# Performance work log

Hardware: AMD Instinct MI355X
Metric: run time of the kernel (lower is better)

Reference implementation:

```python
import jax, jax.numpy as jnp
import numpy as np

NUM_EXPERTS = 8
TOP_K = 2
HIDDEN = 768
INTERMEDIATE = 3072
NUM_TOKENS = 8192


def setup_inputs() -> dict:
    key = jax.random.key(0)
    k0, k1, k2, k3 = jax.random.split(key, 4)
    hidden_states = jax.random.normal(k0, (NUM_TOKENS, HIDDEN), dtype=jnp.float32)
    router_weight = jax.random.normal(k1, (NUM_EXPERTS, HIDDEN), dtype=jnp.float32) * 0.02
    w1 = jax.random.normal(k2, (NUM_EXPERTS, INTERMEDIATE, HIDDEN), dtype=jnp.float32) * 0.02
    w2 = jax.random.normal(k3, (NUM_EXPERTS, HIDDEN, INTERMEDIATE), dtype=jnp.float32) * 0.02
    bias = jnp.zeros((HIDDEN,), dtype=jnp.float32)
    return {"hidden_states": hidden_states, "router_weight": router_weight,
            "w1": w1, "w2": w2, "bias": bias}


def _moe_forward(hidden_states, router_weight, w1, w2, bias):
    T, H = hidden_states.shape
    E = w1.shape[0]
    # Router: ReplicatedLinear(H, E, bias=False)
    logits = hidden_states @ router_weight.T                      # [T, E]
    # fused_topk: softmax over all experts, then top-k, renormalize=False
    probs = jax.nn.softmax(logits, axis=-1)                       # [T, E]
    topk_w, topk_ids = jax.lax.top_k(probs, TOP_K)                # [T, K]
    # per-token per-expert combine weight (top-k ids are distinct)
    gates = jnp.sum(jax.nn.one_hot(topk_ids, E, dtype=probs.dtype) * topk_w[..., None], axis=1)  # [T, E]
    # Expert MLP: y_e = gelu(x @ w1[e].T) @ w2[e].T  (non-gated, activation_without_mul('gelu'))
    out = jnp.zeros_like(hidden_states)
    for e in range(E):  # small fixed expert count
        h = jax.nn.gelu(hidden_states @ w1[e].T, approximate=False)  # [T, I]
        out = out + gates[:, e:e + 1] * (h @ w2[e].T)                # [T, H]
    return out + bias


def reference(hidden_states, router_weight, w1, w2, bias):
    return _moe_forward(hidden_states, router_weight, w1, w2, bias)
```

## Files before the change

kernel.cpp:

```cpp
#include <hip/hip_runtime.h>
#include <hip/hip_bf16.h>
#include <math.h>

#define NT 8192
#define HD 768
#define ID 3072
#define NE 8
#define BK 32
#define MAXB 72
#define ASZ (256 * BK)
#define BSZ (128 * BK)
#define RT_BLOCKS 256
#define CW1_BLOCKS (NE * ID * HD / 4 / 1024)
#define G1_GEMM (MAXB * (ID / 128))
#define CW2_BLOCKS (NE * HD * ID / 4 / 2048)

typedef __bf16 bf16x8 __attribute__((ext_vector_type(8)));
typedef float f32x4 __attribute__((ext_vector_type(4)));

__device__ __forceinline__ unsigned short f2bf(float f) {
    union { float f; unsigned u; } v; v.f = f;
    unsigned r = v.u + 0x7FFFu + ((v.u >> 16) & 1u);
    return (unsigned short)(r >> 16);
}
__device__ __forceinline__ float bf2f(unsigned short b) {
    union { unsigned u; float f; } v; v.u = ((unsigned)b) << 16;
    return v.f;
}
__device__ __forceinline__ unsigned cvt_pk_bf16(float lo, float hi) {
    unsigned r;
    asm("v_cvt_pk_bf16_f32 %0, %1, %2" : "=v"(r) : "v"(lo), "v"(hi));
    return r;
}
__device__ __forceinline__ float gelu_s(float v) {
    float z = v * (1.5957691216057308f + 0.07135481283687945f * v * v);
    float e = __expf(-z);
    return v * __builtin_amdgcn_rcpf(1.0f + e);
}

__device__ __forceinline__ void gload16(const void* g, void* l) {
    auto* lds = reinterpret_cast<__attribute__((address_space(3))) unsigned int*>(
        reinterpret_cast<uintptr_t>(l));
    auto* gp = reinterpret_cast<const __attribute__((address_space(1))) unsigned int*>(
        reinterpret_cast<uintptr_t>(g));
    __builtin_amdgcn_global_load_lds(gp, lds, 16, 0, 0);
}

__device__ __forceinline__ void decode_em(const int* counts, int bsw, int& e, int& m0) {
    e = -1; m0 = 0;
    int s = 0;
#pragma unroll
    for (int q = 0; q < NE; q++) {
        int nb = (counts[q] + 255) >> 8;
        if (bsw >= s && bsw < s + nb) { e = q; m0 = (bsw - s) << 8; }
        s += nb;
    }
}

__global__ void k_front(const float* __restrict__ x, const float* __restrict__ rw,
                        const float4* __restrict__ w1, ushort4* __restrict__ w1b,
                        ushort4* __restrict__ xb4, float* __restrict__ gates,
                        uchar2* __restrict__ choice) {
    __shared__ float rws[NE * HD];
    const int tid = threadIdx.x;
    if (blockIdx.x >= RT_BLOCKS) {
        int base = (blockIdx.x - RT_BLOCKS) * 1024 + tid;
#pragma unroll
        for (int i = 0; i < 4; i++) {
            int idx = base + i * 256;
            float4 a = w1[idx];
            ushort4 ra;
            ra.x = f2bf(a.x); ra.y = f2bf(a.y); ra.z = f2bf(a.z); ra.w = f2bf(a.w);
            w1b[idx] = ra;
        }
        return;
    }
    for (int i = tid; i < NE * HD / 4; i += 256)
        ((float4*)rws)[i] = ((const float4*)rw)[i];
    __syncthreads();
    const int wid = tid >> 6, lane = tid & 63;
    const float4* rws4 = (const float4*)rws;
    for (int it = 0; it < 8; ++it) {
        const int t = blockIdx.x * 32 + wid * 8 + it;
        const float4* xp4 = (const float4*)(x + (size_t)t * HD);
        float acc[NE];
#pragma unroll
        for (int e = 0; e < NE; e++) acc[e] = 0.f;
#pragma unroll
        for (int j = 0; j < HD / 256; j++) {
            float4 v = xp4[lane + 64 * j];
            ushort4 o;
            o.x = f2bf(v.x); o.y = f2bf(v.y); o.z = f2bf(v.z); o.w = f2bf(v.w);
            xb4[(size_t)t * (HD / 4) + lane + 64 * j] = o;
#pragma unroll
            for (int e = 0; e < NE; e++) {
                float4 w = rws4[e * (HD / 4) + lane + 64 * j];
                acc[e] += v.x * w.x + v.y * w.y + v.z * w.z + v.w * w.w;
            }
        }
#pragma unroll
        for (int e = 0; e < NE; e++)
            for (int off = 32; off; off >>= 1) acc[e] += __shfl_xor(acc[e], off);
        if (lane == 0) {
            float mx = acc[0];
#pragma unroll
            for (int e = 1; e < NE; e++) mx = fmaxf(mx, acc[e]);
            float p[NE], s = 0.f;
#pragma unroll
            for (int e = 0; e < NE; e++) { p[e] = __expf(acc[e] - mx); s += p[e]; }
            float inv = 1.f / s;
            int i1 = 0; float b1 = p[0];
#pragma unroll
            for (int e = 1; e < NE; e++) if (p[e] > b1) { b1 = p[e]; i1 = e; }
            int i2 = (i1 == 0) ? 1 : 0; float b2 = p[i2];
#pragma unroll
            for (int e = 0; e < NE; e++) if (e != i1 && p[e] > b2) { b2 = p[e]; i2 = e; }
            choice[t].x = (unsigned char)i1;
            choice[t].y = (unsigned char)i2;
            gates[2 * t] = b1 * inv;
            gates[2 * t + 1] = b2 * inv;
        }
    }
}

__global__ void k_cnt(const uchar2* __restrict__ choice, int* __restrict__ ccnt) {
    const int e = blockIdx.x >> 3, c = blockIdx.x & 7;
    const int tid = threadIdx.x, wid = tid >> 6, lane = tid & 63;
    __shared__ int ws[4];
    int tot = 0;
#pragma unroll
    for (int p = 0; p < 4; p++) {
        int t = c * 1024 + p * 256 + tid;
        uchar2 ch = choice[t];
        bool m = (ch.x == e) || (ch.y == e);
        unsigned long long mask = __ballot(m);
        if (lane == 0) tot += __popcll(mask);
    }
    if (lane == 0) ws[wid] = tot;
    __syncthreads();
    if (tid == 0) ccnt[blockIdx.x] = ws[0] + ws[1] + ws[2] + ws[3];
}

__global__ void k_wr(const uchar2* __restrict__ choice, const int* __restrict__ ccnt,
                     int* __restrict__ lists, int* __restrict__ counts) {
    const int e = blockIdx.x >> 3, c = blockIdx.x & 7;
    const int tid = threadIdx.x, wid = tid >> 6, lane = tid & 63;
    __shared__ int wtot[4];
    __shared__ int running;
    if (tid == 0) {
        int b = 0;
        for (int q = 0; q < c; q++) b += ccnt[e * 8 + q];
        running = b;
        if (c == 7) counts[e] = b + ccnt[e * 8 + 7];
    }
    __syncthreads();
#pragma unroll
    for (int p = 0; p < 4; p++) {
        int t = c * 1024 + p * 256 + tid;
        uchar2 ch = choice[t];
        bool m1 = (ch.x == e), m2 = (ch.y == e);
        bool m = m1 || m2;
        int slot = m1 ? 2 * t : 2 * t + 1;
        unsigned long long mask = __ballot(m);
        int off = __popcll(mask & ((1ULL << lane) - 1ULL));
        if (lane == 0) wtot[wid] = __popcll(mask);
        __syncthreads();
        int base = running;
        for (int w = 0; w < wid; w++) base += wtot[w];
        if (m) lists[e * NT + base + off] = slot;
        __syncthreads();
        if (tid == 0) running += wtot[0] + wtot[1] + wtot[2] + wtot[3];
        __syncthreads();
    }
}


__launch_bounds__(512, 2)
__global__ void k_gemm1(const unsigned short* __restrict__ xb, const unsigned short* __restrict__ w1b,
                        const float4* __restrict__ w2, ushort4* __restrict__ w2b,
                        const int* __restrict__ lists, const int* __restrict__ counts,
                        unsigned short* __restrict__ hbuf) {
    const int tid = threadIdx.x;
    if (blockIdx.x >= G1_GEMM) {
        int base = (blockIdx.x - G1_GEMM) * 2048 + tid;
#pragma unroll
        for (int i = 0; i < 4; i++) {
            int idx = base + i * 512;
            float4 a = w2[idx];
            ushort4 ra;
            ra.x = f2bf(a.x); ra.y = f2bf(a.y); ra.z = f2bf(a.z); ra.w = f2bf(a.w);
            w2b[idx] = ra;
        }
        return;
    }
    const int mi = blockIdx.x % MAXB;
    const int ny = blockIdx.x / MAXB;
    const int bsw = (mi & 7) * (MAXB >> 3) + (mi >> 3);
    int e, m0;
    decode_em(counts, bsw, e, m0);
    if (e < 0) return;
    const int cnt = counts[e];
    const int n0 = ny * 128;
    __shared__ __align__(16) unsigned short As[3 * ASZ];
    __shared__ __align__(16) unsigned short Bs[3 * BSZ];
    __shared__ int slot_s[256];
    const int lane = tid & 63, wid = tid >> 6;
    if (tid < 256) {
        int r = m0 + tid;
        slot_s[tid] = lists[e * NT + (r < cnt ? r : cnt - 1)];
    }
    __syncthreads();

    const int rsub = lane >> 2;
    const int sw = (((lane & 3) ^ ((rsub >> 1) & 3)) * 8);
    const int row0 = wid * 16 + rsub;
    const unsigned short* gA0 = xb + (size_t)(slot_s[row0] >> 1) * HD + sw;
    const unsigned short* gA1 = xb + (size_t)(slot_s[row0 + 128] >> 1) * HD + sw;
    const unsigned short* gB0 = w1b + ((size_t)e * ID + n0 + row0) * HD + sw;
    auto stage = [&](int bf) {
        gload16(gA0, As + bf * ASZ + wid * 512);       gA0 += BK;
        gload16(gA1, As + bf * ASZ + (wid + 8) * 512); gA1 += BK;
        gload16(gB0, Bs + bf * BSZ + wid * 512);       gB0 += BK;
    };

    const int wr = wid >> 1, wc = wid & 1;
    const int l15 = lane & 15, l4 = lane >> 4;
    const int aBase = (wr * 64 + l15) * BK;
    const int bBase = (wc * 64 + l15) * BK;
    const int cs = (l4 ^ ((l15 >> 1) & 3)) * 8;

    f32x4 acc[4][4];
    f32x4 zero = {0.f, 0.f, 0.f, 0.f};
#pragma unroll
    for (int m = 0; m < 4; m++)
#pragma unroll
        for (int n = 0; n < 4; n++) acc[m][n] = zero;

    const int NK = HD / BK;
    stage(0); stage(1);
    int cur = 0, pf = 2;
    for (int kt = 0; kt < NK; ++kt) {
        if (kt + 1 < NK) asm volatile("s_waitcnt vmcnt(3)\ns_barrier" ::: "memory");
        else             asm volatile("s_waitcnt vmcnt(0)\ns_barrier" ::: "memory");
        if (kt + 2 < NK) { stage(pf); pf = (pf == 2) ? 0 : pf + 1; }
        const unsigned short* Ab = As + cur * ASZ;
        const unsigned short* Bb = Bs + cur * BSZ;
        bf16x8 a[4], b[4];
#pragma unroll
        for (int m = 0; m < 4; m++) a[m] = *(const bf16x8*)(Ab + aBase + m * 512 + cs);
#pragma unroll
        for (int n = 0; n < 4; n++) b[n] = *(const bf16x8*)(Bb + bBase + n * 512 + cs);
        __builtin_amdgcn_s_setprio(1);
#pragma unroll
        for (int m = 0; m < 4; m++)
#pragma unroll
            for (int n = 0; n < 4; n++)
                acc[m][n] = __builtin_amdgcn_mfma_f32_16x16x32_bf16(b[n], a[m], acc[m][n], 0, 0, 0);
        __builtin_amdgcn_s_setprio(0);
        cur = (cur == 2) ? 0 : cur + 1;
    }
    const int rj = l4 * 4;
#pragma unroll
    for (int m = 0; m < 4; m++) {
        int lr2 = wr * 64 + m * 16 + l15;
        if (m0 + lr2 < cnt) {
            int slot = slot_s[lr2];
            unsigned short* hp = hbuf + (size_t)slot * ID + n0 + wc * 64 + rj;
#pragma unroll
            for (int n = 0; n < 4; n++) {
                uint2 pk;
                pk.x = cvt_pk_bf16(gelu_s(acc[m][n][0]), gelu_s(acc[m][n][1]));
                pk.y = cvt_pk_bf16(gelu_s(acc[m][n][2]), gelu_s(acc[m][n][3]));
                *(uint2*)(hp + n * 16) = pk;
            }
        }
    }
}

__launch_bounds__(512, 2)
__global__ void k_gemm2(const unsigned short* __restrict__ hbuf, const unsigned short* __restrict__ w2b,
                        const int* __restrict__ lists, const int* __restrict__ counts,
                        const float* __restrict__ gates, unsigned short* __restrict__ pout) {
    const int bsw = (blockIdx.x & 7) * (MAXB >> 3) + (blockIdx.x >> 3);
    int e, m0;
    decode_em(counts, bsw, e, m0);
    if (e < 0) return;
    const int cnt = counts[e];
    const int n0 = blockIdx.y * 128;
    __shared__ __align__(16) unsigned short As[3 * ASZ];
    __shared__ __align__(16) unsigned short Bs[3 * BSZ];
    __shared__ int slot_s[256];
    const int tid = threadIdx.x, lane = tid & 63, wid = tid >> 6;
    if (tid < 256) {
        int r = m0 + tid;
        slot_s[tid] = lists[e * NT + (r < cnt ? r : cnt - 1)];
    }
    __syncthreads();

    const int rsub = lane >> 2;
    const int sw = (((lane & 3) ^ ((rsub >> 1) & 3)) * 8);
    const int row0 = wid * 16 + rsub;
    const unsigned short* gA0 = hbuf + (size_t)slot_s[row0] * ID + sw;
    const unsigned short* gA1 = hbuf + (size_t)slot_s[row0 + 128] * ID + sw;
    const unsigned short* gB0 = w2b + ((size_t)e * HD + n0 + row0) * ID + sw;
    auto stage = [&](int bf) {
        gload16(gA0, As + bf * ASZ + wid * 512);       gA0 += BK;
        gload16(gA1, As + bf * ASZ + (wid + 8) * 512); gA1 += BK;
        gload16(gB0, Bs + bf * BSZ + wid * 512);       gB0 += BK;
    };

    const int wr = wid >> 1, wc = wid & 1;
    const int l15 = lane & 15, l4 = lane >> 4;
    const int aBase = (wr * 64 + l15) * BK;
    const int bBase = (wc * 64 + l15) * BK;
    const int cs = (l4 ^ ((l15 >> 1) & 3)) * 8;

    f32x4 acc[4][4];
    f32x4 zero = {0.f, 0.f, 0.f, 0.f};
#pragma unroll
    for (int m = 0; m < 4; m++)
#pragma unroll
        for (int n = 0; n < 4; n++) acc[m][n] = zero;

    const int NK = ID / BK;
    stage(0); stage(1);
    int cur = 0, pf = 2;
    for (int kt = 0; kt < NK; ++kt) {
        if (kt + 1 < NK) asm volatile("s_waitcnt vmcnt(3)\ns_barrier" ::: "memory");
        else             asm volatile("s_waitcnt vmcnt(0)\ns_barrier" ::: "memory");
        if (kt + 2 < NK) { stage(pf); pf = (pf == 2) ? 0 : pf + 1; }
        const unsigned short* Ab = As + cur * ASZ;
        const unsigned short* Bb = Bs + cur * BSZ;
        bf16x8 a[4], b[4];
#pragma unroll
        for (int m = 0; m < 4; m++) a[m] = *(const bf16x8*)(Ab + aBase + m * 512 + cs);
#pragma unroll
        for (int n = 0; n < 4; n++) b[n] = *(const bf16x8*)(Bb + bBase + n * 512 + cs);
        __builtin_amdgcn_s_setprio(1);
#pragma unroll
        for (int m = 0; m < 4; m++)
#pragma unroll
            for (int n = 0; n < 4; n++)
                acc[m][n] = __builtin_amdgcn_mfma_f32_16x16x32_bf16(b[n], a[m], acc[m][n], 0, 0, 0);
        __builtin_amdgcn_s_setprio(0);
        cur = (cur == 2) ? 0 : cur + 1;
    }
    const int rj = l4 * 4;
#pragma unroll
    for (int m = 0; m < 4; m++) {
        int lr2 = wr * 64 + m * 16 + l15;
        if (m0 + lr2 < cnt) {
            int slot = slot_s[lr2];
            float g = gates[slot];
            unsigned short* pp = pout + (size_t)slot * HD + n0 + wc * 64 + rj;
#pragma unroll
            for (int n = 0; n < 4; n++) {
                uint2 pk;
                pk.x = cvt_pk_bf16(g * acc[m][n][0], g * acc[m][n][1]);
                pk.y = cvt_pk_bf16(g * acc[m][n][2], g * acc[m][n][3]);
                *(uint2*)(pp + n * 16) = pk;
            }
        }
    }
}

__global__ void k_combine(const unsigned short* __restrict__ pout, const float* __restrict__ bias,
                          float4* __restrict__ out) {
    int idx = blockIdx.x * 256 + threadIdx.x;
    int t = idx / (HD / 4);
    int c = idx - t * (HD / 4);
    ushort4 a = ((const ushort4*)pout)[(size_t)t * (2 * HD / 4) + c];
    ushort4 b = ((const ushort4*)pout)[(size_t)t * (2 * HD / 4) + HD / 4 + c];
    float4 bb = ((const float4*)bias)[c];
    float4 r;
    r.x = bf2f(a.x) + bf2f(b.x) + bb.x;
    r.y = bf2f(a.y) + bf2f(b.y) + bb.y;
    r.z = bf2f(a.z) + bf2f(b.z) + bb.z;
    r.w = bf2f(a.w) + bf2f(b.w) + bb.w;
    out[idx] = r;
}

extern "C" void kernel_launch(void* const* d_in, const int* in_sizes, int n_in,
                              void* d_out, int out_size, void* d_ws, size_t ws_size,
                              hipStream_t stream) {
    const float* x    = (const float*)d_in[0];
    const float* rw   = (const float*)d_in[1];
    const float* w1   = (const float*)d_in[2];
    const float* w2   = (const float*)d_in[3];
    const float* bias = (const float*)d_in[4];
    float* out = (float*)d_out;

    char* ws = (char*)d_ws;
    size_t off = 0;
    auto alloc = [&](size_t bytes) -> char* {
        char* p = ws + off;
        off += (bytes + 255) & ~(size_t)255;
        return p;
    };
    int*            counts = (int*)alloc(NE * 4);
    int*            ccnt   = (int*)alloc(NE * 8 * 4);
    int*            lists  = (int*)alloc((size_t)NE * NT * 4);
    float*          gates  = (float*)alloc((size_t)NT * 2 * 4);
    uchar2*         choice = (uchar2*)alloc((size_t)NT * 2);
    unsigned short* xb     = (unsigned short*)alloc((size_t)NT * HD * 2);
    unsigned short* w1b    = (unsigned short*)alloc((size_t)NE * ID * HD * 2);
    unsigned short* w2b    = (unsigned short*)alloc((size_t)NE * HD * ID * 2);
    unsigned short* hbuf   = (unsigned short*)alloc((size_t)NT * 2 * ID * 2);
    unsigned short* pout   = (unsigned short*)alloc((size_t)NT * 2 * HD * 2);

    k_front<<<dim3(RT_BLOCKS + CW1_BLOCKS), dim3(256), 0, stream>>>(
        x, rw, (const float4*)w1, (ushort4*)w1b, (ushort4*)xb, gates, choice);
    k_cnt<<<dim3(64), dim3(256), 0, stream>>>(choice, ccnt);
    k_wr<<<dim3(64), dim3(256), 0, stream>>>(choice, ccnt, lists, counts);
    k_gemm1<<<dim3(G1_GEMM + CW2_BLOCKS), dim3(512), 0, stream>>>(
        xb, w1b, (const float4*)w2, (ushort4*)w2b, lists, counts, hbuf);
    k_gemm2<<<dim3(MAXB, HD / 128), dim3(512), 0, stream>>>(hbuf, w2b, lists, counts, gates, pout);
    k_combine<<<dim3(NT * HD / 4 / 256), dim3(256), 0, stream>>>(pout, bias, (float4*)out);
}
```

Baseline: 262.7 us.

## Enlarge gemm2 tile to 256x256 with split-phase 4-stage pipeline

```diff
diff --git a/kernel.cpp b/kernel.cpp
--- a/kernel.cpp
+++ b/kernel.cpp
@@ -10,6 +10,7 @@
 #define MAXB 72
 #define ASZ (256 * BK)
 #define BSZ (128 * BK)
+#define TSZ (256 * BK)
 #define RT_BLOCKS 256
 #define CW1_BLOCKS (NE * ID * HD / 4 / 1024)
 #define G1_GEMM (MAXB * (ID / 128))
@@ -174,7 +175,6 @@
     }
 }
 
-
 __launch_bounds__(512, 2)
 __global__ void k_gemm1(const unsigned short* __restrict__ xb, const unsigned short* __restrict__ w1b,
                         const float4* __restrict__ w2, ushort4* __restrict__ w2b,
@@ -286,9 +286,9 @@
     decode_em(counts, bsw, e, m0);
     if (e < 0) return;
     const int cnt = counts[e];
-    const int n0 = blockIdx.y * 128;
-    __shared__ __align__(16) unsigned short As[3 * ASZ];
-    __shared__ __align__(16) unsigned short Bs[3 * BSZ];
+    const int n0 = blockIdx.y * 256;
+    __shared__ __align__(16) unsigned short As[4 * TSZ];
+    __shared__ __align__(16) unsigned short Bs[4 * TSZ];
     __shared__ int slot_s[256];
     const int tid = threadIdx.x, lane = tid & 63, wid = tid >> 6;
     if (tid < 256) {
@@ -303,39 +303,41 @@
     const unsigned short* gA0 = hbuf + (size_t)slot_s[row0] * ID + sw;
     const unsigned short* gA1 = hbuf + (size_t)slot_s[row0 + 128] * ID + sw;
     const unsigned short* gB0 = w2b + ((size_t)e * HD + n0 + row0) * ID + sw;
-    auto stage = [&](int bf) {
-        gload16(gA0, As + bf * ASZ + wid * 512);       gA0 += BK;
-        gload16(gA1, As + bf * ASZ + (wid + 8) * 512); gA1 += BK;
-        gload16(gB0, Bs + bf * BSZ + wid * 512);       gB0 += BK;
+    const unsigned short* gB1 = w2b + ((size_t)e * HD + n0 + row0 + 128) * ID + sw;
+    auto stageA = [&](int bf) {
+        gload16(gA0, As + bf * TSZ + wid * 512);       gA0 += BK;
+        gload16(gA1, As + bf * TSZ + (wid + 8) * 512); gA1 += BK;
     };
-
-    const int wr = wid >> 1, wc = wid & 1;
+    auto stageB = [&](int bf) {
+        gload16(gB0, Bs + bf * TSZ + wid * 512);       gB0 += BK;
+        gload16(gB1, Bs + bf * TSZ + (wid + 8) * 512); gB1 += BK;
+    };
+
+    const int wr = wid >> 2, wc = wid & 3;
     const int l15 = lane & 15, l4 = lane >> 4;
-    const int aBase = (wr * 64 + l15) * BK;
+    const int aBase = (wr * 128 + l15) * BK;
     const int bBase = (wc * 64 + l15) * BK;
     const int cs = (l4 ^ ((l15 >> 1) & 3)) * 8;
 
-    f32x4 acc[4][4];
+    f32x4 acc[8][4];
     f32x4 zero = {0.f, 0.f, 0.f, 0.f};
 #pragma unroll
-    for (int m = 0; m < 4; m++)
+    for (int m = 0; m < 8; m++)
 #pragma unroll
         for (int n = 0; n < 4; n++) acc[m][n] = zero;
 
     const int NK = ID / BK;
-    stage(0); stage(1);
-    int cur = 0, pf = 2;
-    for (int kt = 0; kt < NK; ++kt) {
-        if (kt + 1 < NK) asm volatile("s_waitcnt vmcnt(3)\ns_barrier" ::: "memory");
-        else             asm volatile("s_waitcnt vmcnt(0)\ns_barrier" ::: "memory");
-        if (kt + 2 < NK) { stage(pf); pf = (pf == 2) ? 0 : pf + 1; }
-        const unsigned short* Ab = As + cur * ASZ;
-        const unsigned short* Bb = Bs + cur * BSZ;
-        bf16x8 a[4], b[4];
+    stageA(0); stageB(0); stageA(1); stageB(1);
+    asm volatile("s_waitcnt vmcnt(4)\ns_barrier" ::: "memory");
+    for (int st = 0; st < NK; ++st) {
+        const unsigned short* Ab = As + (st & 3) * TSZ;
+        const unsigned short* Bb = Bs + (st & 3) * TSZ;
+        bf16x8 b[4], a[4];
+#pragma unroll
+        for (int n = 0; n < 4; n++) b[n] = *(const bf16x8*)(Bb + bBase + n * 512 + cs);
 #pragma unroll
         for (int m = 0; m < 4; m++) a[m] = *(const bf16x8*)(Ab + aBase + m * 512 + cs);
-#pragma unroll
-        for (int n = 0; n < 4; n++) b[n] = *(const bf16x8*)(Bb + bBase + n * 512 + cs);
+        if (st + 2 < NK) stageA((st + 2) & 3);
         __builtin_amdgcn_s_setprio(1);
 #pragma unroll
         for (int m = 0; m < 4; m++)
@@ -343,12 +345,25 @@
             for (int n = 0; n < 4; n++)
                 acc[m][n] = __builtin_amdgcn_mfma_f32_16x16x32_bf16(b[n], a[m], acc[m][n], 0, 0, 0);
         __builtin_amdgcn_s_setprio(0);
-        cur = (cur == 2) ? 0 : cur + 1;
+        asm volatile("s_barrier" ::: "memory");
+        bf16x8 a2[4];
+#pragma unroll
+        for (int m = 0; m < 4; m++) a2[m] = *(const bf16x8*)(Ab + aBase + (m + 4) * 512 + cs);
+        if (st + 2 < NK) stageB((st + 2) & 3);
+        __builtin_amdgcn_s_setprio(1);
+#pragma unroll
+        for (int m = 0; m < 4; m++)
+#pragma unroll
+            for (int n = 0; n < 4; n++)
+                acc[m + 4][n] = __builtin_amdgcn_mfma_f32_16x16x32_bf16(b[n], a2[m], acc[m + 4][n], 0, 0, 0);
+        __builtin_amdgcn_s_setprio(0);
+        if (st + 2 < NK) asm volatile("s_waitcnt vmcnt(4)\ns_barrier" ::: "memory");
+        else             asm volatile("s_waitcnt vmcnt(0)\ns_barrier" ::: "memory");
     }
     const int rj = l4 * 4;
 #pragma unroll
-    for (int m = 0; m < 4; m++) {
-        int lr2 = wr * 64 + m * 16 + l15;
+    for (int m = 0; m < 8; m++) {
+        int lr2 = wr * 128 + m * 16 + l15;
         if (m0 + lr2 < cnt) {
             int slot = slot_s[lr2];
             float g = gates[slot];
@@ -414,6 +429,6 @@
     k_wr<<<dim3(64), dim3(256), 0, stream>>>(choice, ccnt, lists, counts);
     k_gemm1<<<dim3(G1_GEMM + CW2_BLOCKS), dim3(512), 0, stream>>>(
         xb, w1b, (const float4*)w2, (ushort4*)w2b, lists, counts, hbuf);
-    k_gemm2<<<dim3(MAXB, HD / 128), dim3(512), 0, stream>>>(hbuf, w2b, lists, counts, gates, pout);
+    k_gemm2<<<dim3(MAXB, HD / 256), dim3(512), 0, stream>>>(hbuf, w2b, lists, counts, gates, pout);
     k_combine<<<dim3(NT * HD / 4 / 256), dim3(256), 0, stream>>>(pout, bias, (float4*)out);
 }
```

Result: faster. 257.2 us (median of 2 runs) (-2.1%).
